# Optimization experiments

Hardware: AMD Instinct MI355X
Metric: run time of the kernel (lower is better)

## Reference

```python
import jax, jax.numpy as jnp
import numpy as np

B, T, D_IN = 4, 4096, 1024
H, DK, DV, D_MODEL = 16, 64, 64, 1024
EPS = 1e-6


def setup_inputs() -> dict:
    key = jax.random.key(0)
    ks = jax.random.split(key, 11)
    s_in = 1.0 / np.sqrt(D_IN)
    s_o = 1.0 / np.sqrt(H * DV)
    return {
        "query": jax.random.normal(ks[0], (B, T, D_IN), jnp.float32),
        "key": jax.random.normal(ks[1], (B, T, D_IN), jnp.float32),
        "value": jax.random.normal(ks[2], (B, T, D_IN), jnp.float32),
        "Wq": jax.random.normal(ks[3], (D_IN, H * DK), jnp.float32) * s_in,
        "bq": jnp.zeros((H * DK,), jnp.float32),
        "Wk": jax.random.normal(ks[4], (D_IN, H * DK), jnp.float32) * s_in,
        "bk": jnp.zeros((H * DK,), jnp.float32),
        "Wv": jax.random.normal(ks[5], (D_IN, H * DV), jnp.float32) * s_in,
        "bv": jnp.zeros((H * DV,), jnp.float32),
        "Wo": jax.random.normal(ks[6], (H * DV, D_MODEL), jnp.float32) * s_o,
        "bo": jnp.zeros((D_MODEL,), jnp.float32),
    }


def _phi(x):
    # ELU(x) + 1 feature map (positive kernel feature)
    return jax.nn.elu(x) + 1.0


def reference(query, key, value, Wq, bq, Wk, bk, Wv, bv, Wo, bo):
    b, t, _ = query.shape
    q = _phi(query @ Wq + bq).reshape(b, t, H, DK)   # [B,T,H,DK]
    k = _phi(key @ Wk + bk).reshape(b, t, H, DK)     # [B,T,H,DK]
    v = (value @ Wv + bv).reshape(b, t, H, DV)       # [B,T,H,DV]
    # KV accumulation over time: [B,H,DV,DK]
    kv = jnp.einsum('bthd,bthk->bhkd', k, v)
    # normalizer: q . sum_t(k)  -> [B,T,H]
    norm = 1.0 / (jnp.einsum('bthd,bhd->bth', q, k.sum(axis=1)) + EPS)
    attn = jnp.einsum('bthd,bhkd,bth->bthk', q, kv, norm)  # [B,T,H,DV]
    attn = attn.reshape(b, t, H * DV)
    return attn @ Wo + bo
```

## Files before the change

kernel.cpp:

```cpp
#include <hip/hip_runtime.h>

typedef __bf16 bf16;
typedef bf16 bf16x2 __attribute__((ext_vector_type(2)));
typedef bf16 bf16x8 __attribute__((ext_vector_type(8)));
typedef float f32x4 __attribute__((ext_vector_type(4)));

#define B_ 4
#define T_ 4096
#define H_ 16
#define DK_ 64
#define DV_ 64
#define DMODEL_ 1024
#define M_ (B_ * T_)
#define EPS_ 1e-6f

#define BARX()  asm volatile("s_barrier" ::: "memory")
#define LGKM0() asm volatile("s_waitcnt lgkmcnt(0)" ::: "memory")

__device__ __forceinline__ void async_ld16(const void* g, void* l) {
    __builtin_amdgcn_global_load_lds(
        (const __attribute__((address_space(1))) unsigned int*)g,
        (__attribute__((address_space(3))) unsigned int*)l,
        16, 0, 0);
}

struct TPtrs { const float* s[4]; bf16* d[4]; };

__global__ void transpose4(TPtrs p) {
    __shared__ bf16 t[32][33];
    const float* src = p.s[blockIdx.z];
    bf16*        dst = p.d[blockIdx.z];
    const int tx = threadIdx.x, ty = threadIdx.y;
    const int x  = blockIdx.x * 32 + tx;
    const int y0 = blockIdx.y * 32 + ty;
#pragma unroll
    for (int i = 0; i < 32; i += 8)
        t[ty + i][tx] = (bf16)src[(size_t)(y0 + i) * 1024 + x];
    __syncthreads();
    const int xo = blockIdx.y * 32 + tx;
    const int yo = blockIdx.x * 32 + ty;
#pragma unroll
    for (int i = 0; i < 32; i += 8)
        dst[(size_t)(yo + i) * 1024 + xo] = t[tx][ty + i];
}

__global__ __launch_bounds__(256) void cvt_kernel(
    const float* __restrict__ src, bf16* __restrict__ dst)
{
    const size_t i = (size_t)blockIdx.x * 256 + threadIdx.x;
    const float4* s = (const float4*)src + 2 * i;
    float4 a = s[0];
    float4 b = s[1];
    bf16x8 h;
    h[0] = (bf16)a.x; h[1] = (bf16)a.y; h[2] = (bf16)a.z; h[3] = (bf16)a.w;
    h[4] = (bf16)b.x; h[5] = (bf16)b.y; h[6] = (bf16)b.z; h[7] = (bf16)b.w;
    *(bf16x8*)(dst + 8 * i) = h;
}


__device__ __forceinline__ void stage_half(
    const bf16* __restrict__ G, int base_rc, int K,
    char* lds_op_buf, int t, int h, int w, int lane)
{
    const int r8   = lane >> 3;
    const int row  = h * 128 + w * 8 + r8;
    const int cole = (((lane & 7) ^ r8) << 3);
    const bf16* g = G + (size_t)(base_rc + row) * K + t * 64 + cole;
    char* l = lds_op_buf + h * 16384 + w * 1024;
    async_ld16(g, l);
    async_ld16(g + (size_t)64 * K, l + 8192);
}

template<int G>
__device__ __forceinline__ void read_a4(bf16x8 (&aF)[4][2], const char* ab,
                                        int arow, int fq, int l7) {
#pragma unroll
    for (int i = 0; i < 4; ++i)
#pragma unroll
        for (int ks = 0; ks < 2; ++ks)
            aF[i][ks] = *(const bf16x8*)(ab
                + (arow + (G * 4 + i) * 16) * 128
                + ((((ks << 2) + fq) ^ l7) << 4));
}

template<int JP>
__device__ __forceinline__ void read_b2(bf16x8 (&bF)[4][2], const char* bb,
                                        int brow, int fq, int l7) {
#pragma unroll
    for (int j = 0; j < 2; ++j)
#pragma unroll
        for (int ks = 0; ks < 2; ++ks)
            bF[JP * 2 + j][ks] = *(const bf16x8*)(bb
                + (brow + (JP * 2 + j) * 16) * 128
                + ((((ks << 2) + fq) ^ l7) << 4));
}

template<int G, int JP>
__device__ __forceinline__ void mfma_q(f32x4 (&acc)[8][4],
                                       const bf16x8 (&aF)[4][2],
                                       const bf16x8 (&bF)[4][2]) {
#pragma unroll
    for (int i = 0; i < 4; ++i)
#pragma unroll
        for (int j = 0; j < 2; ++j)
#pragma unroll
            for (int ks = 0; ks < 2; ++ks)
                acc[G * 4 + i][JP * 2 + j] =
                    __builtin_amdgcn_mfma_f32_16x16x32_bf16(
                        aF[i][ks], bF[JP * 2 + j][ks],
                        acc[G * 4 + i][JP * 2 + j], 0, 0, 0);
}

template<int ACT, int OUTMODE>
__global__ __launch_bounds__(512, 2) void gemm256_kernel(
    const bf16* __restrict__ A, const bf16* __restrict__ Bt,
    const float* __restrict__ bias, void* __restrict__ Cout,
    const bf16* __restrict__ KV2,
    int M, int N, int K)
{
    __shared__ f32x4 smem4[8192];
    char* smem = (char*)smem4;
    char* Ab0 = smem;
    char* Ab1 = smem + 32768;
    char* Bb0 = smem + 65536;
    char* Bb1 = smem + 98304;

    const int tid  = threadIdx.x;
    const int w    = tid >> 6, lane = tid & 63;
    const int wrow = w >> 2,  wcol = w & 3;
    const int fr = lane & 15, fq = lane >> 4, l7 = lane & 7;
    const int arow = wrow * 128 + fr;
    const int brow = wcol * 64 + fr;

    const int nwg  = gridDim.x * gridDim.y;
    const int flat = blockIdx.y * gridDim.x + blockIdx.x;
    const int swz  = (flat & 7) * (nwg >> 3) + (flat >> 3);
    const int n0   = (swz % gridDim.x) * 256;
    const int m0   = (swz / gridDim.x) * 256;

    const int KT = K >> 6;

    f32x4  acc[8][4] = {};
    bf16x8 aF[4][2], bF[4][2];

    stage_half(Bt, n0, K, Bb0, 0, 0, w, lane);
    stage_half(Bt, n0, K, Bb0, 0, 1, w, lane);
    stage_half(A,  m0, K, Ab0, 0, 0, w, lane);
    stage_half(A,  m0, K, Ab0, 0, 1, w, lane);
    stage_half(Bt, n0, K, Bb1, 1, 0, w, lane);
    stage_half(Bt, n0, K, Bb1, 1, 1, w, lane);
    stage_half(A,  m0, K, Ab1, 1, 0, w, lane);
    stage_half(A,  m0, K, Ab1, 1, 1, w, lane);
    asm volatile("s_waitcnt vmcnt(8)" ::: "memory");
    BARX();

    for (int it = 0; it < (KT >> 1); ++it) {
        const int  t0   = it * 2, t1 = t0 + 1;
        const bool more = (it < (KT >> 1) - 1);

        read_a4<0>(aF, Ab0, arow, fq, l7);
        read_b2<0>(bF, Bb0, brow, fq, l7);
        asm volatile("s_waitcnt lgkmcnt(8)" ::: "memory");
        BARX(); LGKM0();
        __builtin_amdgcn_s_setprio(1);
        mfma_q<0, 0>(acc, aF, bF);
        __builtin_amdgcn_s_setprio(0);
        BARX();

        read_b2<1>(bF, Bb0, brow, fq, l7);
        BARX(); LGKM0();
        __builtin_amdgcn_s_setprio(1);
        mfma_q<0, 1>(acc, aF, bF);
        __builtin_amdgcn_s_setprio(0);
        BARX();

        read_a4<1>(aF, Ab0, arow, fq, l7);
        if (more) {
            stage_half(Bt, n0, K, Bb0, t0 + 2, 0, w, lane);
            stage_half(Bt, n0, K, Bb0, t0 + 2, 1, w, lane);
        }
        BARX(); LGKM0();
        __builtin_amdgcn_s_setprio(1);
        mfma_q<1, 0>(acc, aF, bF);
        __builtin_amdgcn_s_setprio(0);
        BARX();

        if (more) {
            stage_half(A, m0, K, Ab0, t0 + 2, 0, w, lane);
            stage_half(A, m0, K, Ab0, t0 + 2, 1, w, lane);
            asm volatile("s_waitcnt vmcnt(8)" ::: "memory");
        } else {
            asm volatile("s_waitcnt vmcnt(0)" ::: "memory");
        }
        BARX();
        __builtin_amdgcn_s_setprio(1);
        mfma_q<1, 1>(acc, aF, bF);
        __builtin_amdgcn_s_setprio(0);
        BARX();

        read_a4<0>(aF, Ab1, arow, fq, l7);
        read_b2<0>(bF, Bb1, brow, fq, l7);
        asm volatile("s_waitcnt lgkmcnt(8)" ::: "memory");
        BARX(); LGKM0();
        __builtin_amdgcn_s_setprio(1);
        mfma_q<0, 0>(acc, aF, bF);
        __builtin_amdgcn_s_setprio(0);
        BARX();

        read_b2<1>(bF, Bb1, brow, fq, l7);
        BARX(); LGKM0();
        __builtin_amdgcn_s_setprio(1);
        mfma_q<0, 1>(acc, aF, bF);
        __builtin_amdgcn_s_setprio(0);
        BARX();

        read_a4<1>(aF, Ab1, arow, fq, l7);
        if (more) {
            stage_half(Bt, n0, K, Bb1, t1 + 2, 0, w, lane);
            stage_half(Bt, n0, K, Bb1, t1 + 2, 1, w, lane);
        }
        BARX(); LGKM0();
        __builtin_amdgcn_s_setprio(1);
        mfma_q<1, 0>(acc, aF, bF);
        __builtin_amdgcn_s_setprio(0);
        BARX();

        if (more) {
            stage_half(A, m0, K, Ab1, t1 + 2, 0, w, lane);
            stage_half(A, m0, K, Ab1, t1 + 2, 1, w, lane);
            asm volatile("s_waitcnt vmcnt(8)" ::: "memory");
        }
        BARX();
        __builtin_amdgcn_s_setprio(1);
        mfma_q<1, 1>(acc, aF, bF);
        __builtin_amdgcn_s_setprio(0);
        BARX();
    }

    const size_t Ns = (size_t)N;
    if constexpr (OUTMODE == 2) {
        __syncthreads();
        char* eb = smem;
#pragma unroll
        for (int g = 0; g < 8; ++g)
#pragma unroll
            for (int j = 0; j < 4; ++j) {
                const int n = wcol * 64 + j * 16 + fr;
                const float bb = bias[n0 + n];
#pragma unroll
                for (int r = 0; r < 4; ++r) {
                    float x = acc[g][j][r] + bb;
                    if (ACT) x = (x > 0.0f) ? (x + 1.0f) : __expf(x);
                    const int m = wrow * 128 + g * 16 + fq * 4 + r;
                    *(bf16*)(eb + n * 512
                        + ((((m >> 3) ^ (n & 7)) << 4) | ((m & 7) << 1)))
                        = (bf16)x;
                }
            }
        __syncthreads();
        bf16* Cp = (bf16*)Cout;
#pragma unroll
        for (int o = 0; o < 16; ++o) {
            const int n    = (tid >> 5) + o * 16;
            const int mblk = tid & 31;
            bf16x8 v = *(const bf16x8*)(eb + n * 512
                        + ((mblk ^ (n & 7)) << 4));
            *(bf16x8*)(Cp + (size_t)(n0 + n) * M + m0 + mblk * 8) = v;
        }
    } else if constexpr (OUTMODE == 3) {
        __syncthreads();
        char* qb = smem + w * 16384;
#pragma unroll
        for (int g = 0; g < 8; ++g)
#pragma unroll
            for (int j = 0; j < 4; ++j) {
                const int cq = j * 16 + fr;
                const float bb = bias[n0 + wcol * 64 + cq];
#pragma unroll
                for (int r = 0; r < 4; ++r) {
                    float x = acc[g][j][r] + bb;
                    x = (x > 0.0f) ? (x + 1.0f) : __expf(x);
                    const int row = g * 16 + fq * 4 + r;
                    *(bf16*)(qb + row * 128
                        + ((((cq >> 3) ^ (row & 7)) << 4) | ((cq & 7) << 1)))
                        = (bf16)x;
                }
            }
        __syncthreads();

        const int hw = (n0 >> 6) + wcol;
        const int bh = ((m0 >> 12) << 4) + hw;
        const bf16* kvp2 = KV2 + (size_t)bh * 6144;
        bf16x8 bO[6][2];
#pragma unroll
        for (int jj = 0; jj < 6; ++jj)
#pragma unroll
            for (int ks = 0; ks < 2; ++ks)
                bO[jj][ks] = *(const bf16x8*)(kvp2
                    + (jj * 16 + fr) * 64 + ks * 32 + fq * 8);

        bf16* Cp = (bf16*)Cout;
#pragma unroll
        for (int g = 0; g < 8; ++g) {
            bf16x8 aq[2];
#pragma unroll
            for (int ks = 0; ks < 2; ++ks)
                aq[ks] = *(const bf16x8*)(qb + (g * 16 + fr) * 128
                    + ((((ks << 2) + fq) ^ l7) << 4));
            f32x4 o[6] = {};
#pragma unroll
            for (int ks = 0; ks < 2; ++ks)
#pragma unroll
                for (int jj = 0; jj < 6; ++jj)
                    o[jj] = __builtin_amdgcn_mfma_f32_16x16x32_bf16(
                        aq[ks], bO[jj][ks], o[jj], 0, 0, 0);
#pragma unroll
            for (int r = 0; r < 4; ++r) {
                const float nrm = 1.0f / (o[4][r] + o[5][r] + EPS_);
                const size_t row = (size_t)(m0 + wrow * 128 + g * 16
                                            + fq * 4 + r);
#pragma unroll
                for (int jj = 0; jj < 4; ++jj)
                    Cp[row * 1024 + n0 + wcol * 64 + jj * 16 + fr]
                        = (bf16)(o[jj][r] * nrm);
            }
        }
    } else {
#pragma unroll
        for (int g = 0; g < 8; ++g) {
#pragma unroll
            for (int j = 0; j < 4; ++j) {
                const int col = n0 + wcol * 64 + j * 16 + fr;
                const float bb = bias[col];
                const int row0 = m0 + wrow * 128 + g * 16 + fq * 4;
#pragma unroll
                for (int r = 0; r < 4; ++r) {
                    float x = acc[g][j][r] + bb;
                    if (ACT) x = (x > 0.0f) ? (x + 1.0f) : __expf(x);
                    if (OUTMODE == 1)
                        ((float*)Cout)[(size_t)(row0 + r) * Ns + col] = x;
                    else
                        ((bf16*)Cout)[(size_t)(row0 + r) * Ns + col] = (bf16)x;
                }
            }
        }
    }
}

__global__ __launch_bounds__(256) void kv_partial_kernel(
    const bf16* __restrict__ KT, const bf16* __restrict__ VT,
    float* __restrict__ kv_part, float* __restrict__ ksum_part)
{
    const int bh = blockIdx.y, b = bh >> 4, h = bh & 15;
    const int tc = blockIdx.x;
    __shared__ char lds[32768];

    const int tid = threadIdx.x, wv = tid >> 6, lane = tid & 63;
    const int fr = lane & 15, fq = lane >> 4, l7 = lane & 7;

    const int r1 = wv * 8 + (lane >> 3);
    const int c1 = ((lane & 7) ^ (r1 & 7)) << 3;
    const size_t g1 = (size_t)(h * 64 + r1) * M_ + (size_t)b * T_ + c1;
    const size_t g2 = g1 + (size_t)32 * M_;
    const int dstoff = (wv * 64 + lane) * 16;

    f32x4 acc[4] = {};
    float ksa = 0.0f;
    const int rk = tid >> 2, qk = tid & 3;

    {
        const size_t mo = (size_t)tc * 512;
        async_ld16(VT + g1 + mo, lds + dstoff);
        async_ld16(VT + g2 + mo, lds + 4096 + dstoff);
        async_ld16(KT + g1 + mo, lds + 8192 + dstoff);
        async_ld16(KT + g2 + mo, lds + 12288 + dstoff);
    }
    for (int it = 0; it < 8; ++it) {
        char* cur = lds + (it & 1) * 16384;
        char* nxt = lds + ((it & 1) ^ 1) * 16384;
        if (it < 7) {
            const size_t mo = (size_t)tc * 512 + (it + 1) * 64;
            async_ld16(VT + g1 + mo, nxt + dstoff);
            async_ld16(VT + g2 + mo, nxt + 4096 + dstoff);
            async_ld16(KT + g1 + mo, nxt + 8192 + dstoff);
            async_ld16(KT + g2 + mo, nxt + 12288 + dstoff);
            asm volatile("s_waitcnt vmcnt(4)" ::: "memory");
        } else {
            asm volatile("s_waitcnt vmcnt(0)" ::: "memory");
        }
        BARX();
        const char* Vb = cur;
        const char* Kb = cur + 8192;
#pragma unroll
        for (int ks = 0; ks < 2; ++ks) {
            bf16x8 av = *(const bf16x8*)(Vb + (wv * 16 + fr) * 128
                        + ((((ks << 2) + fq) ^ l7) << 4));
#pragma unroll
            for (int j = 0; j < 4; ++j) {
                bf16x8 bk = *(const bf16x8*)(Kb + (j * 16 + fr) * 128
                            + ((((ks << 2) + fq) ^ l7) << 4));
                acc[j] = __builtin_amdgcn_mfma_f32_16x16x32_bf16(
                    av, bk, acc[j], 0, 0, 0);
            }
        }
        {
            bf16x8 s0 = *(const bf16x8*)(Kb + rk * 128 + (((2 * qk) ^ (rk & 7)) << 4));
            bf16x8 s1 = *(const bf16x8*)(Kb + rk * 128 + (((2 * qk + 1) ^ (rk & 7)) << 4));
#pragma unroll
            for (int e = 0; e < 8; ++e) ksa += (float)s0[e] + (float)s1[e];
        }
        BARX();
    }

    float* kvp = kv_part + ((size_t)tc * 64 + bh) * 4096;
#pragma unroll
    for (int j = 0; j < 4; ++j)
#pragma unroll
        for (int r = 0; r < 4; ++r)
            kvp[(wv * 16 + fq * 4 + r) * 64 + j * 16 + fr] = acc[j][r];

    float s = ksa;
    s += __shfl_xor(s, 1);
    s += __shfl_xor(s, 2);
    if (qk == 0) ksum_part[((size_t)tc * 64 + bh) * 64 + rk] = s;
}

__global__ __launch_bounds__(256) void kv_reduce_kernel(
    const float* __restrict__ kv_part, const float* __restrict__ ksum_part,
    bf16* __restrict__ kvb2)
{
    const int bh = blockIdx.x;
    const int tid = threadIdx.x;
    bf16* out = kvb2 + (size_t)bh * 6144;
    for (int e = tid; e < 4096; e += 256) {
        float s = 0.0f;
#pragma unroll
        for (int tc = 0; tc < 8; ++tc)
            s += kv_part[((size_t)tc * 64 + bh) * 4096 + e];
        out[e] = (bf16)s;
    }
    if (tid < 64) {
        float s = 0.0f;
#pragma unroll
        for (int tc = 0; tc < 8; ++tc)
            s += ksum_part[((size_t)tc * 64 + bh) * 64 + tid];
        const bf16 hi = (bf16)s;
        const bf16 lo = (bf16)(s - (float)hi);
#pragma unroll
        for (int i = 0; i < 16; ++i) {
            out[(64 + i) * 64 + tid] = hi;
            out[(80 + i) * 64 + tid] = lo;
        }
    }
}

extern "C" void kernel_launch(void* const* d_in, const int* in_sizes, int n_in,
                              void* d_out, int out_size, void* d_ws, size_t ws_size,
                              hipStream_t stream) {
    const float* query = (const float*)d_in[0];
    const float* key_  = (const float*)d_in[1];
    const float* value = (const float*)d_in[2];
    const float* Wq = (const float*)d_in[3];
    const float* bq = (const float*)d_in[4];
    const float* Wk = (const float*)d_in[5];
    const float* bk = (const float*)d_in[6];
    const float* Wv = (const float*)d_in[7];
    const float* bv = (const float*)d_in[8];
    const float* Wo = (const float*)d_in[9];
    const float* bo = (const float*)d_in[10];

    char* ws = (char*)d_ws;
    char* out8 = (char*)d_out;
    const size_t MB = 1024 * 1024;
    bf16* WqT = (bf16*)(ws + 0 * MB);
    bf16* WkT = (bf16*)(ws + 2 * MB);
    bf16* WvT = (bf16*)(ws + 4 * MB);
    bf16* WoT = (bf16*)(ws + 6 * MB);
    bf16* CVT = (bf16*)(ws + 8 * MB);
    float* kv_part   = (float*)(ws + 40 * MB);
    float* ksum_part = (float*)(ws + 48 * MB);

    bf16* KTg  = (bf16*)out8;
    bf16* VTg  = (bf16*)(out8 + 32 * MB);
    bf16* Qcvt = (bf16*)out8;
    bf16* kvb2 = (bf16*)(out8 + 32 * MB);
    bf16* ATTN = CVT;

    TPtrs tp;
    tp.s[0] = Wq;  tp.s[1] = Wk;  tp.s[2] = Wv;  tp.s[3] = Wo;
    tp.d[0] = WqT; tp.d[1] = WkT; tp.d[2] = WvT; tp.d[3] = WoT;
    transpose4<<<dim3(32, 32, 4), dim3(32, 8, 1), 0, stream>>>(tp);

    const int CVT_BLOCKS = M_ * 1024 / 8 / 256;
    const dim3 G256(4, 64);

    cvt_kernel<<<CVT_BLOCKS, 256, 0, stream>>>(key_, CVT);
    gemm256_kernel<1, 2><<<G256, 512, 0, stream>>>(CVT, WkT, bk, KTg, nullptr, M_, 1024, 1024);

    cvt_kernel<<<CVT_BLOCKS, 256, 0, stream>>>(value, CVT);
    gemm256_kernel<0, 2><<<G256, 512, 0, stream>>>(CVT, WvT, bv, VTg, nullptr, M_, 1024, 1024);

    kv_partial_kernel<<<dim3(8, 64), 256, 0, stream>>>(KTg, VTg, kv_part, ksum_part);
    kv_reduce_kernel<<<dim3(64), 256, 0, stream>>>(kv_part, ksum_part, kvb2);

    cvt_kernel<<<CVT_BLOCKS, 256, 0, stream>>>(query, Qcvt);
    gemm256_kernel<1, 3><<<G256, 512, 0, stream>>>(Qcvt, WqT, bq, ATTN, kvb2, M_, 1024, 1024);

    gemm256_kernel<0, 1><<<G256, 512, 0, stream>>>(ATTN, WoT, bo, (float*)d_out, nullptr, M_, 1024, 1024);
}
```

Measured before the change: 404.6 us.

## Fuse fp32-to-bf16 input conversion into GEMM A-operand staging

Removes the three standalone cvt kernels and instead has the projection GEMMs load fp32 activations into registers, convert them to bf16, and write them swizzled into LDS. This drops a full write and re-read of a 32MB bf16 copy per input plus extra launches. The cost is twice the global bytes for the A tile inside the GEMM, more registers, and synchronous register-staged writes in place of async global-to-LDS loads, which may hurt the pipelining and occupancy of the main loop.

```diff
diff --git a/kernel.cpp b/kernel.cpp
--- a/kernel.cpp
+++ b/kernel.cpp
@@ -42,19 +42,6 @@
 #pragma unroll
     for (int i = 0; i < 32; i += 8)
         dst[(size_t)(yo + i) * 1024 + xo] = t[tx][ty + i];
-}
-
-__global__ __launch_bounds__(256) void cvt_kernel(
-    const float* __restrict__ src, bf16* __restrict__ dst)
-{
-    const size_t i = (size_t)blockIdx.x * 256 + threadIdx.x;
-    const float4* s = (const float4*)src + 2 * i;
-    float4 a = s[0];
-    float4 b = s[1];
-    bf16x8 h;
-    h[0] = (bf16)a.x; h[1] = (bf16)a.y; h[2] = (bf16)a.z; h[3] = (bf16)a.w;
-    h[4] = (bf16)b.x; h[5] = (bf16)b.y; h[6] = (bf16)b.z; h[7] = (bf16)b.w;
-    *(bf16x8*)(dst + 8 * i) = h;
 }
 
 
@@ -71,6 +58,42 @@
     async_ld16(g + (size_t)64 * K, l + 8192);
 }
 
+struct af32regs { float4 v[8]; };
+
+__device__ __forceinline__ void issue_a_f32(
+    const float* __restrict__ Af, int m0, int K, int t, int w, int lane,
+    af32regs& R)
+{
+    const int r8 = lane >> 3, c = lane & 7;
+    const float* g = Af + (size_t)(m0 + w * 8 + r8) * K + t * 64 + c * 8;
+#pragma unroll
+    for (int h = 0; h < 2; ++h) {
+        const float* gh = g + (size_t)(h * 128) * K;
+        R.v[h * 4 + 0] = *(const float4*)(gh);
+        R.v[h * 4 + 1] = *(const float4*)(gh + 4);
+        R.v[h * 4 + 2] = *(const float4*)(gh + (size_t)64 * K);
+        R.v[h * 4 + 3] = *(const float4*)(gh + (size_t)64 * K + 4);
+    }
+}
+
+__device__ __forceinline__ void write_a(char* Abuf, int w, int lane,
+                                        const af32regs& R)
+{
+    const int r8 = lane >> 3, c = lane & 7;
+#pragma unroll
+    for (int h = 0; h < 2; ++h)
+#pragma unroll
+        for (int rr = 0; rr < 2; ++rr) {
+            const int row = h * 128 + w * 8 + r8 + rr * 64;
+            const float4 a = R.v[h * 4 + rr * 2];
+            const float4 b = R.v[h * 4 + rr * 2 + 1];
+            bf16x8 o;
+            o[0] = (bf16)a.x; o[1] = (bf16)a.y; o[2] = (bf16)a.z; o[3] = (bf16)a.w;
+            o[4] = (bf16)b.x; o[5] = (bf16)b.y; o[6] = (bf16)b.z; o[7] = (bf16)b.w;
+            *(bf16x8*)(Abuf + row * 128 + ((c ^ r8) << 4)) = o;
+        }
+}
+
 template<int G>
 __device__ __forceinline__ void read_a4(bf16x8 (&aF)[4][2], const char* ab,
                                         int arow, int fq, int l7) {
@@ -111,9 +134,10 @@
                         acc[G * 4 + i][JP * 2 + j], 0, 0, 0);
 }
 
-template<int ACT, int OUTMODE>
+template<int ACT, int OUTMODE, int AF32>
 __global__ __launch_bounds__(512, 2) void gemm256_kernel(
-    const bf16* __restrict__ A, const bf16* __restrict__ Bt,
+    const bf16* __restrict__ A, const float* __restrict__ Af32,
+    const bf16* __restrict__ Bt,
     const float* __restrict__ bias, void* __restrict__ Cout,
     const bf16* __restrict__ KV2,
     int M, int N, int K)
@@ -142,16 +166,31 @@
 
     f32x4  acc[8][4] = {};
     bf16x8 aF[4][2], bF[4][2];
-
-    stage_half(Bt, n0, K, Bb0, 0, 0, w, lane);
-    stage_half(Bt, n0, K, Bb0, 0, 1, w, lane);
-    stage_half(A,  m0, K, Ab0, 0, 0, w, lane);
-    stage_half(A,  m0, K, Ab0, 0, 1, w, lane);
-    stage_half(Bt, n0, K, Bb1, 1, 0, w, lane);
-    stage_half(Bt, n0, K, Bb1, 1, 1, w, lane);
-    stage_half(A,  m0, K, Ab1, 1, 0, w, lane);
-    stage_half(A,  m0, K, Ab1, 1, 1, w, lane);
-    asm volatile("s_waitcnt vmcnt(8)" ::: "memory");
+    af32regs RA;
+
+    if constexpr (AF32) {
+        issue_a_f32(Af32, m0, K, 0, w, lane, RA);
+        stage_half(Bt, n0, K, Bb0, 0, 0, w, lane);
+        stage_half(Bt, n0, K, Bb0, 0, 1, w, lane);
+        asm volatile("s_waitcnt vmcnt(4)" ::: "memory");
+        write_a(Ab0, w, lane, RA);
+        issue_a_f32(Af32, m0, K, 1, w, lane, RA);
+        stage_half(Bt, n0, K, Bb1, 1, 0, w, lane);
+        stage_half(Bt, n0, K, Bb1, 1, 1, w, lane);
+        asm volatile("s_waitcnt vmcnt(4)" ::: "memory");
+        write_a(Ab1, w, lane, RA);
+        LGKM0();
+    } else {
+        stage_half(Bt, n0, K, Bb0, 0, 0, w, lane);
+        stage_half(Bt, n0, K, Bb0, 0, 1, w, lane);
+        stage_half(A,  m0, K, Ab0, 0, 0, w, lane);
+        stage_half(A,  m0, K, Ab0, 0, 1, w, lane);
+        stage_half(Bt, n0, K, Bb1, 1, 0, w, lane);
+        stage_half(Bt, n0, K, Bb1, 1, 1, w, lane);
+        stage_half(A,  m0, K, Ab1, 1, 0, w, lane);
+        stage_half(A,  m0, K, Ab1, 1, 1, w, lane);
+        asm volatile("s_waitcnt vmcnt(8)" ::: "memory");
+    }
     BARX();
 
     for (int it = 0; it < (KT >> 1); ++it) {
@@ -168,6 +207,7 @@
         BARX();
 
         read_b2<1>(bF, Bb0, brow, fq, l7);
+        if (AF32 && more) issue_a_f32(Af32, m0, K, t0 + 2, w, lane, RA);
         BARX(); LGKM0();
         __builtin_amdgcn_s_setprio(1);
         mfma_q<0, 1>(acc, aF, bF);
@@ -186,9 +226,15 @@
         BARX();
 
         if (more) {
-            stage_half(A, m0, K, Ab0, t0 + 2, 0, w, lane);
-            stage_half(A, m0, K, Ab0, t0 + 2, 1, w, lane);
-            asm volatile("s_waitcnt vmcnt(8)" ::: "memory");
+            if constexpr (AF32) {
+                asm volatile("s_waitcnt vmcnt(4)" ::: "memory");
+                write_a(Ab0, w, lane, RA);
+                LGKM0();
+            } else {
+                stage_half(A, m0, K, Ab0, t0 + 2, 0, w, lane);
+                stage_half(A, m0, K, Ab0, t0 + 2, 1, w, lane);
+                asm volatile("s_waitcnt vmcnt(8)" ::: "memory");
+            }
         } else {
             asm volatile("s_waitcnt vmcnt(0)" ::: "memory");
         }
@@ -208,6 +254,7 @@
         BARX();
 
         read_b2<1>(bF, Bb1, brow, fq, l7);
+        if (AF32 && more) issue_a_f32(Af32, m0, K, t1 + 2, w, lane, RA);
         BARX(); LGKM0();
         __builtin_amdgcn_s_setprio(1);
         mfma_q<0, 1>(acc, aF, bF);
@@ -226,9 +273,15 @@
         BARX();
 
         if (more) {
-            stage_half(A, m0, K, Ab1, t1 + 2, 0, w, lane);
-            stage_half(A, m0, K, Ab1, t1 + 2, 1, w, lane);
-            asm volatile("s_waitcnt vmcnt(8)" ::: "memory");
+            if constexpr (AF32) {
+                asm volatile("s_waitcnt vmcnt(4)" ::: "memory");
+                write_a(Ab1, w, lane, RA);
+                LGKM0();
+            } else {
+                stage_half(A, m0, K, Ab1, t1 + 2, 0, w, lane);
+                stage_half(A, m0, K, Ab1, t1 + 2, 1, w, lane);
+                asm volatile("s_waitcnt vmcnt(8)" ::: "memory");
+            }
         }
         BARX();
         __builtin_amdgcn_s_setprio(1);
@@ -476,35 +529,33 @@
     bf16* WkT = (bf16*)(ws + 2 * MB);
     bf16* WvT = (bf16*)(ws + 4 * MB);
     bf16* WoT = (bf16*)(ws + 6 * MB);
-    bf16* CVT = (bf16*)(ws + 8 * MB);
+    bf16* ATTN = (bf16*)(ws + 8 * MB);
     float* kv_part   = (float*)(ws + 40 * MB);
     float* ksum_part = (float*)(ws + 48 * MB);
 
     bf16* KTg  = (bf16*)out8;
     bf16* VTg  = (bf16*)(out8 + 32 * MB);
-    bf16* Qcvt = (bf16*)out8;
     bf16* kvb2 = (bf16*)(out8 + 32 * MB);
-    bf16* ATTN = CVT;
 
     TPtrs tp;
     tp.s[0] = Wq;  tp.s[1] = Wk;  tp.s[2] = Wv;  tp.s[3] = Wo;
     tp.d[0] = WqT; tp.d[1] = WkT; tp.d[2] = WvT; tp.d[3] = WoT;
     transpose4<<<dim3(32, 32, 4), dim3(32, 8, 1), 0, stream>>>(tp);
 
-    const int CVT_BLOCKS = M_ * 1024 / 8 / 256;
     const dim3 G256(4, 64);
 
-    cvt_kernel<<<CVT_BLOCKS, 256, 0, stream>>>(key_, CVT);
-    gemm256_kernel<1, 2><<<G256, 512, 0, stream>>>(CVT, WkT, bk, KTg, nullptr, M_, 1024, 1024);
-
-    cvt_kernel<<<CVT_BLOCKS, 256, 0, stream>>>(value, CVT);
-    gemm256_kernel<0, 2><<<G256, 512, 0, stream>>>(CVT, WvT, bv, VTg, nullptr, M_, 1024, 1024);
+    gemm256_kernel<1, 2, 1><<<G256, 512, 0, stream>>>(
+        nullptr, key_, WkT, bk, KTg, nullptr, M_, 1024, 1024);
+
+    gemm256_kernel<0, 2, 1><<<G256, 512, 0, stream>>>(
+        nullptr, value, WvT, bv, VTg, nullptr, M_, 1024, 1024);
 
     kv_partial_kernel<<<dim3(8, 64), 256, 0, stream>>>(KTg, VTg, kv_part, ksum_part);
     kv_reduce_kernel<<<dim3(64), 256, 0, stream>>>(kv_part, ksum_part, kvb2);
 
-    cvt_kernel<<<CVT_BLOCKS, 256, 0, stream>>>(query, Qcvt);
-    gemm256_kernel<1, 3><<<G256, 512, 0, stream>>>(Qcvt, WqT, bq, ATTN, kvb2, M_, 1024, 1024);
-
-    gemm256_kernel<0, 1><<<G256, 512, 0, stream>>>(ATTN, WoT, bo, (float*)d_out, nullptr, M_, 1024, 1024);
-}
+    gemm256_kernel<1, 3, 1><<<G256, 512, 0, stream>>>(
+        nullptr, query, WqT, bq, ATTN, kvb2, M_, 1024, 1024);
+
+    gemm256_kernel<0, 1, 0><<<G256, 512, 0, stream>>>(
+        ATTN, nullptr, WoT, bo, (float*)d_out, nullptr, M_, 1024, 1024);
+}
```

Result: slower. 470.5 us (+16.3%).
